# Kernel tuning notes

Measured on AMD Instinct MI355X. Metric: run time of the kernel, lower is better.

## Reference

```python
import jax, jax.numpy as jnp
import numpy as np

HEAD_DIM = 64

def setup_inputs() -> dict:
    key = jax.random.key(0)
    k1, k2, k3, k4 = jax.random.split(key, 4)
    B, S, D, H = 8, 2048, 1024, HEAD_DIM
    x = jax.random.normal(k1, (B, S, D), dtype=jnp.float32)
    scale = 1.0 / np.sqrt(D)
    W_q = jax.random.normal(k2, (H, D), dtype=jnp.float32) * scale
    W_k = jax.random.normal(k3, (H, D), dtype=jnp.float32) * scale
    W_v = jax.random.normal(k4, (H, D), dtype=jnp.float32) * scale
    return {"input_embeddings": x, "W_q": W_q, "W_k": W_k, "W_v": W_v}

def reference(input_embeddings, W_q, W_k, W_v):
    # Linear(model_dim, head_dim, bias=False): y = x @ W.T
    q = jnp.einsum('bsd,hd->bsh', input_embeddings, W_q)
    k = jnp.einsum('bsd,hd->bsh', input_embeddings, W_k)
    v = jnp.einsum('bsd,hd->bsh', input_embeddings, W_v)
    scores = jnp.einsum('bqh,bkh->bqk', q, k) / jnp.sqrt(jnp.float32(HEAD_DIM))
    S = scores.shape[-1]
    causal = jnp.tril(jnp.ones((S, S), dtype=bool))  # [S,S]
    scores = jnp.where(causal, scores, -jnp.inf)
    attn = jax.nn.softmax(scores, axis=-1)
    # dropout p=0.0 (eval-equivalent): identity
    return jnp.einsum('bqk,bkh->bqh', attn, v)
```

## Files before the change

kernel.cpp:

```cpp
#include <hip/hip_runtime.h>
#include <hip/hip_bf16.h>

typedef __bf16 bf16x8 __attribute__((ext_vector_type(8)));
typedef __bf16 bf16x4 __attribute__((ext_vector_type(4)));
typedef float  f32x4  __attribute__((ext_vector_type(4)));

#define NB  8
#define SEQ 2048
#define DM  1024
#define HD  64

#define WAITV5 asm volatile("s_waitcnt vmcnt(5)" ::: "memory")
#define WAITV0 asm volatile("s_waitcnt vmcnt(0)" ::: "memory")

__device__ __forceinline__ void gll16(const void* g, void* l) {
    __builtin_amdgcn_global_load_lds(
        (const __attribute__((address_space(1))) unsigned int*)g,
        (__attribute__((address_space(3))) unsigned int*)l, 16, 0, 0);
}

__global__ void k_convw(const float* __restrict__ Wq, const float* __restrict__ Wk,
                        const float* __restrict__ Wv, __bf16* __restrict__ Wb) {
    int idx = blockIdx.x * blockDim.x + threadIdx.x;
    int e = idx * 4;
    const float* src;
    if (e < 65536)       src = Wq + e;
    else if (e < 131072) src = Wk + (e - 65536);
    else                 src = Wv + (e - 131072);
    float4 v = *reinterpret_cast<const float4*>(src);
    bf16x4 o;
    o[0] = (__bf16)v.x; o[1] = (__bf16)v.y; o[2] = (__bf16)v.z; o[3] = (__bf16)v.w;
    *reinterpret_cast<bf16x4*>(Wb + e) = o;
}

__launch_bounds__(512, 4)
__global__ void k_proj(const float* __restrict__ X, const __bf16* __restrict__ Wb,
                       __bf16* __restrict__ Qb, __bf16* __restrict__ Kb,
                       __bf16* __restrict__ Vt) {
    __shared__ __align__(16) float  Xs[2][4096];
    __shared__ __align__(16) __bf16 Ws[2][12288];
    const int tid = threadIdx.x;
    const int w = tid >> 6, l = tid & 63;
    const int lr = l & 15, lg = l >> 4;
    const int wm = w >> 2, wn = w & 3;
    const int m0 = blockIdx.x * 64;

    const float* xsrc[2];
    #pragma unroll
    for (int j = 0; j < 2; ++j) {
        int u = w * 128 + j * 64 + l;
        int r_ = u >> 4, c_ = u & 15;
        xsrc[j] = X + (size_t)(m0 + r_) * DM + (c_ ^ (r_ & 15)) * 4;
    }
    const __bf16* wsrc[3];
    #pragma unroll
    for (int j = 0; j < 3; ++j) {
        int u = w * 192 + j * 64 + l;
        int r_ = u >> 3, c_ = u & 7;
        wsrc[j] = Wb + (size_t)r_ * DM + (c_ ^ (r_ & 7)) * 8;
    }

    f32x4 acc[2][3];
    #pragma unroll
    for (int mt = 0; mt < 2; ++mt)
        #pragma unroll
        for (int ct = 0; ct < 3; ++ct)
            acc[mt][ct] = f32x4{0.f, 0.f, 0.f, 0.f};

    int abase[2], bbase[3];
    #pragma unroll
    for (int mt = 0; mt < 2; ++mt) abase[mt] = (wm * 32 + mt * 16 + lr) * 64;
    #pragma unroll
    for (int ct = 0; ct < 3; ++ct) bbase[ct] = ((wn * 3 + ct) * 16 + lr) * 64;

    #pragma unroll
    for (int j = 0; j < 2; ++j) gll16(xsrc[j], &Xs[0][w * 512 + j * 256]);
    #pragma unroll
    for (int j = 0; j < 3; ++j) gll16(wsrc[j], &Ws[0][w * 1536 + j * 512]);

    #pragma unroll
    for (int t = 0; t < 16; ++t) {
        const int cur = t & 1;
        __builtin_amdgcn_s_barrier();
        if (t + 1 < 16) {
            #pragma unroll
            for (int j = 0; j < 2; ++j)
                gll16(xsrc[j] + (size_t)(t + 1) * 64, &Xs[cur ^ 1][w * 512 + j * 256]);
            #pragma unroll
            for (int j = 0; j < 3; ++j)
                gll16(wsrc[j] + (size_t)(t + 1) * 64, &Ws[cur ^ 1][w * 1536 + j * 512]);
            WAITV5;
        } else {
            WAITV0;
        }
        const float*  Xp = &Xs[cur][0];
        const __bf16* Wp = &Ws[cur][0];
        #pragma unroll
        for (int ks = 0; ks < 2; ++ks) {
            bf16x8 af[2];
            #pragma unroll
            for (int mt = 0; mt < 2; ++mt) {
                f32x4 a0 = *reinterpret_cast<const f32x4*>(Xp + abase[mt] + ((ks * 8 + lg * 2)     ^ lr) * 4);
                f32x4 a1 = *reinterpret_cast<const f32x4*>(Xp + abase[mt] + ((ks * 8 + lg * 2 + 1) ^ lr) * 4);
                #pragma unroll
                for (int j = 0; j < 4; ++j) { af[mt][j] = (__bf16)a0[j]; af[mt][4 + j] = (__bf16)a1[j]; }
            }
            #pragma unroll
            for (int ct = 0; ct < 3; ++ct) {
                bf16x8 bf = *reinterpret_cast<const bf16x8*>(
                    Wp + bbase[ct] + (((ks * 4 + lg) ^ (lr & 7)) * 8));
                #pragma unroll
                for (int mt = 0; mt < 2; ++mt)
                    acc[mt][ct] = __builtin_amdgcn_mfma_f32_16x16x32_bf16(
                        af[mt], bf, acc[mt][ct], 0, 0, 0);
            }
        }
    }

    #pragma unroll
    for (int mt = 0; mt < 2; ++mt) {
        const int rowbase = m0 + wm * 32 + mt * 16 + lg * 4;
        #pragma unroll
        for (int ct = 0; ct < 3; ++ct) {
            const int ntile = wn * 3 + ct;
            const int mtx = ntile >> 2;
            const int d = (ntile & 3) * 16 + lr;
            if (mtx == 0) {
                #pragma unroll
                for (int r = 0; r < 4; ++r)
                    Qb[(size_t)(rowbase + r) * HD + d] = (__bf16)(acc[mt][ct][r] * 0.18033688f);
            } else if (mtx == 1) {
                #pragma unroll
                for (int r = 0; r < 4; ++r)
                    Kb[(size_t)(rowbase + r) * HD + d] = (__bf16)acc[mt][ct][r];
            } else {
                int bb = rowbase >> 11;
                int s0 = rowbase & 2047;
                bf16x4 vv;
                #pragma unroll
                for (int r = 0; r < 4; ++r) vv[r] = (__bf16)acc[mt][ct][r];
                *reinterpret_cast<bf16x4*>(Vt + ((size_t)bb * HD + d) * SEQ + s0) = vv;
            }
        }
    }
}

__launch_bounds__(512)
__global__ void k_attn(const __bf16* __restrict__ Qb, const __bf16* __restrict__ Kb,
                       const __bf16* __restrict__ Vt, __bf16* __restrict__ Opart,
                       float* __restrict__ ML, int T, int NC) {
    const int bid = blockIdx.x;
    const int b = bid / (16 * NC);
    const int rem = bid - b * 16 * NC;
    const int qt2 = rem / NC;
    const int c = rem - qt2 * NC;
    const int kmax = 2 * qt2 + 1;
    if (c * T > kmax) return;
    const int kt0 = c * T;
    const int nt = min(T, kmax + 1 - kt0);
    const int q0 = qt2 * 128;

    __shared__ __align__(16) __bf16 Ks[64][72];
    __shared__ __align__(16) __bf16 Vs[64][72];
    __shared__ __align__(16) __bf16 Ps[128][72];
    const int tid = threadIdx.x;
    const int w = tid >> 6, l = tid & 63;
    const int lr = l & 15, lg = l >> 4;
    const __bf16* Qp = Qb + (size_t)b * SEQ * HD;
    const __bf16* Kp = Kb + (size_t)b * SEQ * HD;
    const __bf16* Vp = Vt + (size_t)b * HD * SEQ;

    const int srow = tid >> 3, sc8 = (tid & 7) * 8;
    const int myq = q0 + 16 * w + lr;

    bf16x8 qa[2];
    #pragma unroll
    for (int ks = 0; ks < 2; ++ks)
        qa[ks] = *reinterpret_cast<const bf16x8*>(
            Qp + (size_t)myq * HD + ks * 32 + lg * 8);

    bf16x8 kpre, vpre;
    {
        const int k0 = kt0 * 64;
        kpre = *reinterpret_cast<const bf16x8*>(Kp + (size_t)(k0 + srow) * HD + sc8);
        vpre = *reinterpret_cast<const bf16x8*>(Vp + (size_t)srow * SEQ + k0 + sc8);
    }

    f32x4 oacc[4];
    #pragma unroll
    for (int r = 0; r < 4; ++r) oacc[r] = f32x4{0.f, 0.f, 0.f, 0.f};
    float m = -1e30f, lsum = 0.f;

    for (int it = 0; it < nt; ++it) {
        const int kt = kt0 + it;
        const int k0 = kt * 64;
        __syncthreads();
        *reinterpret_cast<bf16x8*>(&Ks[srow][sc8]) = kpre;
        *reinterpret_cast<bf16x8*>(&Vs[srow][sc8]) = vpre;
        __syncthreads();
        if (it + 1 < nt) {
            const int k0n = k0 + 64;
            kpre = *reinterpret_cast<const bf16x8*>(Kp + (size_t)(k0n + srow) * HD + sc8);
            vpre = *reinterpret_cast<const bf16x8*>(Vp + (size_t)srow * SEQ + k0n + sc8);
        }

        if (k0 > q0 + 16 * w + 15) continue;

        f32x4 sacc[4];
        #pragma unroll
        for (int t = 0; t < 4; ++t) sacc[t] = f32x4{0.f, 0.f, 0.f, 0.f};
        #pragma unroll
        for (int ks = 0; ks < 2; ++ks) {
            #pragma unroll
            for (int t = 0; t < 4; ++t) {
                bf16x8 kf = *reinterpret_cast<const bf16x8*>(&Ks[16 * t + lr][ks * 32 + lg * 8]);
                sacc[t] = __builtin_amdgcn_mfma_f32_16x16x32_bf16(kf, qa[ks], sacc[t], 0, 0, 0);
            }
        }

        float pmax = -1e30f;
        if (k0 + 63 > q0 + 16 * w) {
            #pragma unroll
            for (int t = 0; t < 4; ++t)
                #pragma unroll
                for (int r = 0; r < 4; ++r) {
                    float v = sacc[t][r];
                    if ((k0 + 16 * t + lg * 4 + r) > myq) v = -1e30f;
                    sacc[t][r] = v;
                    pmax = fmaxf(pmax, v);
                }
        } else {
            #pragma unroll
            for (int t = 0; t < 4; ++t)
                #pragma unroll
                for (int r = 0; r < 4; ++r) pmax = fmaxf(pmax, sacc[t][r]);
        }
        pmax = fmaxf(pmax, __shfl_xor(pmax, 16));
        pmax = fmaxf(pmax, __shfl_xor(pmax, 32));

        if (!__all(pmax <= m + 12.f)) {
            float mnew = fmaxf(m, pmax);
            float fsc = exp2f(m - mnew);
            m = mnew;
            lsum *= fsc;
            #pragma unroll
            for (int r = 0; r < 4; ++r) {
                float fq = __shfl(fsc, (l & 48) + lg * 4 + r);
                #pragma unroll
                for (int t2 = 0; t2 < 4; ++t2) oacc[t2][r] *= fq;
            }
        }

        float rs = 0.f;
        #pragma unroll
        for (int t = 0; t < 4; ++t)
            #pragma unroll
            for (int r = 0; r < 4; ++r) {
                float p = exp2f(sacc[t][r] - m);
                sacc[t][r] = p;
                rs += p;
            }
        rs += __shfl_xor(rs, 16);
        rs += __shfl_xor(rs, 32);
        lsum += rs;

        #pragma unroll
        for (int t = 0; t < 4; ++t) {
            bf16x4 pv;
            #pragma unroll
            for (int r = 0; r < 4; ++r) pv[r] = (__bf16)sacc[t][r];
            *reinterpret_cast<bf16x4*>(&Ps[16 * w + lr][16 * t + lg * 4]) = pv;
        }

        #pragma unroll
        for (int ks = 0; ks < 2; ++ks) {
            bf16x8 pa = *reinterpret_cast<const bf16x8*>(&Ps[16 * w + lr][ks * 32 + lg * 8]);
            #pragma unroll
            for (int t2 = 0; t2 < 4; ++t2) {
                bf16x8 vb = *reinterpret_cast<const bf16x8*>(&Vs[16 * t2 + lr][ks * 32 + lg * 8]);
                oacc[t2] = __builtin_amdgcn_mfma_f32_16x16x32_bf16(pa, vb, oacc[t2], 0, 0, 0);
            }
        }
    }

    const size_t slot = (size_t)bid;
    __bf16* op = Opart + slot * 8192;
    #pragma unroll
    for (int t2 = 0; t2 < 4; ++t2)
        #pragma unroll
        for (int r = 0; r < 4; ++r)
            op[(16 * w + lg * 4 + r) * 64 + 16 * t2 + lr] = (__bf16)oacc[t2][r];
    if (lg == 0) {
        float* ml = ML + slot * 256;
        int row = 16 * w + lr;
        ml[row * 2]     = m;
        ml[row * 2 + 1] = lsum;
    }
}

__launch_bounds__(512)
__global__ void k_merge(const __bf16* __restrict__ Opart, const float* __restrict__ ML,
                        float* __restrict__ Out, int T, int NC) {
    const int bq2 = blockIdx.x >> 1;
    const int half = blockIdx.x & 1;
    const int qt2 = bq2 & 15;
    const int nc = (2 * qt2 + 1) / T + 1;
    const int tid = threadIdx.x;
    const int row = tid >> 2;
    const int cg = (tid & 3) * 8 + half * 32;
    const int base = bq2 * NC;

    float M = -1e30f;
    for (int c = 0; c < nc; ++c)
        M = fmaxf(M, ML[(size_t)(base + c) * 256 + row * 2]);

    float L = 0.f;
    f32x4 a0{0,0,0,0}, a1{0,0,0,0};
    for (int c = 0; c < nc; ++c) {
        const float* ml = ML + (size_t)(base + c) * 256 + row * 2;
        float wgt = exp2f(ml[0] - M);
        L += ml[1] * wgt;
        bf16x8 v = *reinterpret_cast<const bf16x8*>(
            Opart + (size_t)(base + c) * 8192 + row * 64 + cg);
        #pragma unroll
        for (int j = 0; j < 4; ++j) {
            a0[j] += wgt * (float)v[j];
            a1[j] += wgt * (float)v[4 + j];
        }
    }
    float inv = 1.f / L;
    #pragma unroll
    for (int j = 0; j < 4; ++j) { a0[j] *= inv; a1[j] *= inv; }
    float* o = Out + ((size_t)bq2 * 128 + row) * 64 + cg;
    *reinterpret_cast<f32x4*>(o)     = a0;
    *reinterpret_cast<f32x4*>(o + 4) = a1;
}

extern "C" void kernel_launch(void* const* d_in, const int* in_sizes, int n_in,
                              void* d_out, int out_size, void* d_ws, size_t ws_size,
                              hipStream_t stream) {
    const float* x  = (const float*)d_in[0];
    const float* wq = (const float*)d_in[1];
    const float* wk = (const float*)d_in[2];
    const float* wv = (const float*)d_in[3];
    char* ws = (char*)d_ws;
    __bf16* Wb = (__bf16*)ws;
    __bf16* Qb = (__bf16*)(ws + 524288);
    __bf16* Kb = (__bf16*)(ws + 524288 + 2097152);
    __bf16* Vt = (__bf16*)(ws + 524288 + 2 * 2097152);
    const size_t base = 524288 + 3 * 2097152;
    float* out = (float*)d_out;

    int NC = (ws_size >= base + (size_t)(8 * 16 * 4) * 17408) ? 4 : 2;
    int T = 32 / NC;
    const int slots = 8 * 16 * NC;
    float*  ML    = (float*)(ws + base);
    __bf16* Opart = (__bf16*)(ws + base + (size_t)slots * 1024);

    hipLaunchKernelGGL(k_convw, dim3(192), dim3(256), 0, stream, wq, wk, wv, Wb);
    hipLaunchKernelGGL(k_proj,  dim3(256), dim3(512), 0, stream, x, Wb, Qb, Kb, Vt);
    hipLaunchKernelGGL(k_attn,  dim3(8 * 16 * NC), dim3(512), 0, stream,
                       Qb, Kb, Vt, Opart, ML, T, NC);
    hipLaunchKernelGGL(k_merge, dim3(256), dim3(512), 0, stream, Opart, ML, out, T, NC);
}
```

Baseline: 55.02 us.

## Widen attention KV tile from 64 to 128 keys per iteration

Each loop iteration of the attention kernel now stages 128 keys of K and V instead of 64. Each warp computes 8 score MFMA tiles and 4 PV k-steps per iteration, which halves the iteration count, the barriers and the softmax/rescale bookkeeping. The causal bounds and the merge chunk count are recomputed for 128-wide tiles, and shared-memory padding changes. In exchange, the per-warp early skip of fully masked tiles is gone, so some warps on the diagonal tile do masked work. Register and LDS pressure also rise, which may lower occupancy.

```diff
diff --git a/kernel.cpp b/kernel.cpp
--- a/kernel.cpp
+++ b/kernel.cpp
@@ -154,15 +154,14 @@
     const int rem = bid - b * 16 * NC;
     const int qt2 = rem / NC;
     const int c = rem - qt2 * NC;
-    const int kmax = 2 * qt2 + 1;
-    if (c * T > kmax) return;
+    if (c * T > qt2) return;
     const int kt0 = c * T;
-    const int nt = min(T, kmax + 1 - kt0);
+    const int nt = min(T, qt2 + 1 - kt0);
     const int q0 = qt2 * 128;
 
-    __shared__ __align__(16) __bf16 Ks[64][72];
-    __shared__ __align__(16) __bf16 Vs[64][72];
-    __shared__ __align__(16) __bf16 Ps[128][72];
+    __shared__ __align__(16) __bf16 Ks[128][72];
+    __shared__ __align__(16) __bf16 Vs[64][136];
+    __shared__ __align__(16) __bf16 Ps[128][136];
     const int tid = threadIdx.x;
     const int w = tid >> 6, l = tid & 63;
     const int lr = l & 15, lg = l >> 4;
@@ -170,7 +169,10 @@
     const __bf16* Kp = Kb + (size_t)b * SEQ * HD;
     const __bf16* Vp = Vt + (size_t)b * HD * SEQ;
 
-    const int srow = tid >> 3, sc8 = (tid & 7) * 8;
+    const int krow0 = tid >> 3,  kcu0 = tid & 7;
+    const int krow1 = (tid + 512) >> 3, kcu1 = tid & 7;
+    const int vrow0 = tid >> 4,  vcu0 = tid & 15;
+    const int vrow1 = (tid + 512) >> 4, vcu1 = tid & 15;
     const int myq = q0 + 16 * w + lr;
 
     bf16x8 qa[2];
@@ -179,11 +181,13 @@
         qa[ks] = *reinterpret_cast<const bf16x8*>(
             Qp + (size_t)myq * HD + ks * 32 + lg * 8);
 
-    bf16x8 kpre, vpre;
+    bf16x8 kpre[2], vpre[2];
     {
-        const int k0 = kt0 * 64;
-        kpre = *reinterpret_cast<const bf16x8*>(Kp + (size_t)(k0 + srow) * HD + sc8);
-        vpre = *reinterpret_cast<const bf16x8*>(Vp + (size_t)srow * SEQ + k0 + sc8);
+        const int k0 = kt0 * 128;
+        kpre[0] = *reinterpret_cast<const bf16x8*>(Kp + (size_t)(k0 + krow0) * HD + kcu0 * 8);
+        kpre[1] = *reinterpret_cast<const bf16x8*>(Kp + (size_t)(k0 + krow1) * HD + kcu1 * 8);
+        vpre[0] = *reinterpret_cast<const bf16x8*>(Vp + (size_t)vrow0 * SEQ + k0 + vcu0 * 8);
+        vpre[1] = *reinterpret_cast<const bf16x8*>(Vp + (size_t)vrow1 * SEQ + k0 + vcu1 * 8);
     }
 
     f32x4 oacc[4];
@@ -193,35 +197,37 @@
 
     for (int it = 0; it < nt; ++it) {
         const int kt = kt0 + it;
-        const int k0 = kt * 64;
+        const int k0 = kt * 128;
         __syncthreads();
-        *reinterpret_cast<bf16x8*>(&Ks[srow][sc8]) = kpre;
-        *reinterpret_cast<bf16x8*>(&Vs[srow][sc8]) = vpre;
+        *reinterpret_cast<bf16x8*>(&Ks[krow0][kcu0 * 8]) = kpre[0];
+        *reinterpret_cast<bf16x8*>(&Ks[krow1][kcu1 * 8]) = kpre[1];
+        *reinterpret_cast<bf16x8*>(&Vs[vrow0][vcu0 * 8]) = vpre[0];
+        *reinterpret_cast<bf16x8*>(&Vs[vrow1][vcu1 * 8]) = vpre[1];
         __syncthreads();
         if (it + 1 < nt) {
-            const int k0n = k0 + 64;
-            kpre = *reinterpret_cast<const bf16x8*>(Kp + (size_t)(k0n + srow) * HD + sc8);
-            vpre = *reinterpret_cast<const bf16x8*>(Vp + (size_t)srow * SEQ + k0n + sc8);
-        }
-
-        if (k0 > q0 + 16 * w + 15) continue;
-
-        f32x4 sacc[4];
-        #pragma unroll
-        for (int t = 0; t < 4; ++t) sacc[t] = f32x4{0.f, 0.f, 0.f, 0.f};
+            const int k0n = k0 + 128;
+            kpre[0] = *reinterpret_cast<const bf16x8*>(Kp + (size_t)(k0n + krow0) * HD + kcu0 * 8);
+            kpre[1] = *reinterpret_cast<const bf16x8*>(Kp + (size_t)(k0n + krow1) * HD + kcu1 * 8);
+            vpre[0] = *reinterpret_cast<const bf16x8*>(Vp + (size_t)vrow0 * SEQ + k0n + vcu0 * 8);
+            vpre[1] = *reinterpret_cast<const bf16x8*>(Vp + (size_t)vrow1 * SEQ + k0n + vcu1 * 8);
+        }
+
+        f32x4 sacc[8];
+        #pragma unroll
+        for (int t = 0; t < 8; ++t) sacc[t] = f32x4{0.f, 0.f, 0.f, 0.f};
         #pragma unroll
         for (int ks = 0; ks < 2; ++ks) {
             #pragma unroll
-            for (int t = 0; t < 4; ++t) {
+            for (int t = 0; t < 8; ++t) {
                 bf16x8 kf = *reinterpret_cast<const bf16x8*>(&Ks[16 * t + lr][ks * 32 + lg * 8]);
                 sacc[t] = __builtin_amdgcn_mfma_f32_16x16x32_bf16(kf, qa[ks], sacc[t], 0, 0, 0);
             }
         }
 
         float pmax = -1e30f;
-        if (k0 + 63 > q0 + 16 * w) {
-            #pragma unroll
-            for (int t = 0; t < 4; ++t)
+        if (kt == qt2) {
+            #pragma unroll
+            for (int t = 0; t < 8; ++t)
                 #pragma unroll
                 for (int r = 0; r < 4; ++r) {
                     float v = sacc[t][r];
@@ -231,7 +237,7 @@
                 }
         } else {
             #pragma unroll
-            for (int t = 0; t < 4; ++t)
+            for (int t = 0; t < 8; ++t)
                 #pragma unroll
                 for (int r = 0; r < 4; ++r) pmax = fmaxf(pmax, sacc[t][r]);
         }
@@ -253,7 +259,7 @@
 
         float rs = 0.f;
         #pragma unroll
-        for (int t = 0; t < 4; ++t)
+        for (int t = 0; t < 8; ++t)
             #pragma unroll
             for (int r = 0; r < 4; ++r) {
                 float p = exp2f(sacc[t][r] - m);
@@ -265,7 +271,7 @@
         lsum += rs;
 
         #pragma unroll
-        for (int t = 0; t < 4; ++t) {
+        for (int t = 0; t < 8; ++t) {
             bf16x4 pv;
             #pragma unroll
             for (int r = 0; r < 4; ++r) pv[r] = (__bf16)sacc[t][r];
@@ -273,7 +279,7 @@
         }
 
         #pragma unroll
-        for (int ks = 0; ks < 2; ++ks) {
+        for (int ks = 0; ks < 4; ++ks) {
             bf16x8 pa = *reinterpret_cast<const bf16x8*>(&Ps[16 * w + lr][ks * 32 + lg * 8]);
             #pragma unroll
             for (int t2 = 0; t2 < 4; ++t2) {
@@ -304,7 +310,7 @@
     const int bq2 = blockIdx.x >> 1;
     const int half = blockIdx.x & 1;
     const int qt2 = bq2 & 15;
-    const int nc = (2 * qt2 + 1) / T + 1;
+    const int nc = qt2 / T + 1;
     const int tid = threadIdx.x;
     const int row = tid >> 2;
     const int cg = (tid & 3) * 8 + half * 32;
@@ -352,7 +358,7 @@
     float* out = (float*)d_out;
 
     int NC = (ws_size >= base + (size_t)(8 * 16 * 4) * 17408) ? 4 : 2;
-    int T = 32 / NC;
+    int T = 16 / NC;
     const int slots = 8 * 16 * NC;
     float*  ML    = (float*)(ws + base);
     __bf16* Opart = (__bf16*)(ws + base + (size_t)slots * 1024);
```

Result: no change. 54.45 us (-1.0%).
